# Kernel tuning notes

Hardware: AMD Instinct MI355X
Metric: run time of the kernel (lower is better)

The kernel has to match this reference:

```python
import jax, jax.numpy as jnp
import numpy as np

N_NODES = 100000
N_EDGES = 1600000
IN, HID, OUT = 128, 64, 64


def setup_inputs() -> dict:
    key = jax.random.key(0)
    ks = jax.random.split(key, 7)
    features = jax.random.normal(ks[0], (N_NODES, IN), dtype=jnp.float32)
    src = jax.random.randint(ks[1], (N_EDGES,), 0, N_NODES, dtype=jnp.int64)
    dst = jax.random.randint(ks[2], (N_EDGES,), 0, N_NODES, dtype=jnp.int64)
    # glorot-uniform-like init for GraphConv weights
    lim1 = np.sqrt(6.0 / (IN + HID)).astype(np.float32)
    lim2 = np.sqrt(6.0 / (HID + OUT)).astype(np.float32)
    W1 = jax.random.uniform(ks[3], (IN, HID), jnp.float32, -lim1, lim1)
    b1 = jnp.zeros((HID,), jnp.float32)
    W2 = jax.random.uniform(ks[4], (HID, OUT), jnp.float32, -lim2, lim2)
    b2 = jnp.zeros((OUT,), jnp.float32)
    return {"features": features, "src": src, "dst": dst,
            "W1": W1, "b1": b1, "W2": W2, "b2": b2}


def _graph_conv(h, W, b, src, dst, out_norm, in_norm, relu, n_nodes):
    # DGL GraphConv, norm='both':
    #   h_src *= outdeg^{-1/2}; aggregate sum over edges; h_dst *= indeg^{-1/2}
    #   W applied before aggregation if in_feats > out_feats (fewer bytes moved)
    h = h * out_norm[:, None]
    if h.shape[1] > W.shape[1]:
        h = h @ W
        agg = jax.ops.segment_sum(h[src], dst, num_segments=n_nodes)
    else:
        agg = jax.ops.segment_sum(h[src], dst, num_segments=n_nodes)
        agg = agg @ W
    out = agg * in_norm[:, None] + b
    return jax.nn.relu(out) if relu else out


def reference(features, src, dst, W1, b1, W2, b2):
    n_nodes = features.shape[0]
    ones = jnp.ones(src.shape[0], features.dtype)
    out_deg = jnp.maximum(jax.ops.segment_sum(ones, src, num_segments=n_nodes), 1.0)
    in_deg = jnp.maximum(jax.ops.segment_sum(ones, dst, num_segments=n_nodes), 1.0)
    out_norm = jax.lax.rsqrt(out_deg)
    in_norm = jax.lax.rsqrt(in_deg)
    h = _graph_conv(features, W1, b1, src, dst, out_norm, in_norm, True, n_nodes)
    # Dropout(0.5) between layers: identity in eval mode
    h = _graph_conv(h, W2, b2, src, dst, out_norm, in_norm, False, n_nodes)
    return h
```

## Files before the change

### kernel.cpp

```cpp
#include <hip/hip_runtime.h>
#include <hip/hip_fp16.h>

#define NCH 64
#define INF 128
#define PAD 64
#define NPART 8
#define HCHUNK 12500
#define HQ 64

using ivec4 = __attribute__((ext_vector_type(4))) int;
using hvec8 = __attribute__((ext_vector_type(8))) _Float16;
using fvec8 = __attribute__((ext_vector_type(8))) float;
using half8 = __attribute__((ext_vector_type(8))) _Float16;
using f32x4 = __attribute__((ext_vector_type(4))) float;

__global__ __launch_bounds__(256) void k_histo(const int* __restrict__ src,
                                               int* __restrict__ ohist, int nE, int nN) {
    __shared__ int cnt[HCHUNK];
    const int p = blockIdx.x & (NPART - 1);
    const int q = blockIdx.x >> 3;
    const int lo = p * HCHUNK;
    const int hi = (lo + HCHUNK < nN) ? lo + HCHUNK : nN;
    for (int i = threadIdx.x; i < HCHUNK; i += 256) cnt[i] = 0;
    __syncthreads();
    const int nE4 = nE >> 2;
    const int b0 = (int)(((long)q * nE4) / HQ);
    const int b1 = (int)(((long)(q + 1) * nE4) / HQ);
    for (int i = b0 + threadIdx.x; i < b1; i += 256) {
        ivec4 s4 = __builtin_nontemporal_load(((const ivec4*)src) + i);
#pragma unroll
        for (int j = 0; j < 4; ++j) {
            int s = s4[j];
            if (s >= lo && s < hi) atomicAdd(&cnt[s - lo], 1);
        }
    }
    if (q == 0 && threadIdx.x < (nE & 3)) {
        int s = src[(nE4 << 2) + threadIdx.x];
        if (s >= lo && s < hi) atomicAdd(&cnt[s - lo], 1);
    }
    __syncthreads();
    int* dstp = ohist + (long)blockIdx.x * HCHUNK;
    for (int i = threadIdx.x; i < HCHUNK; i += 256) dstp[i] = cnt[i];
}

__global__ void k_osum(const int* __restrict__ ohist, float* __restrict__ onorm, int nN) {
    int n = blockIdx.x * blockDim.x + threadIdx.x;
    if (n >= nN) return;
    int p = n / HCHUNK, i = n - p * HCHUNK;
    int s = 0;
#pragma unroll 4
    for (int q = 0; q < HQ; ++q)
        s += ohist[(long)((q << 3) | p) * HCHUNK + i];
    onorm[n] = rsqrtf(fmaxf((float)s, 1.0f));
}

__global__ __launch_bounds__(256) void k_build2(
    const int* __restrict__ src, const int* __restrict__ dst,
    int* __restrict__ indeg, int* __restrict__ ell, int nE, int chunk)
{
    const int part = blockIdx.x & (NPART - 1);
    const int lo = part * chunk;
    const int hi = lo + chunk;
    const int setid = blockIdx.x >> 3;
    const int nset = gridDim.x >> 3;
    const int nE4 = nE >> 2;

    int t = setid * 256 + threadIdx.x;
    int stride = nset * 256;
    for (int i = t; i < nE4; i += stride) {
        ivec4 s4 = __builtin_nontemporal_load(((const ivec4*)src) + i);
        ivec4 d4 = __builtin_nontemporal_load(((const ivec4*)dst) + i);
#pragma unroll
        for (int j = 0; j < 4; ++j) {
            int d = d4[j];
            if (d >= lo && d < hi) {
                int pos = atomicAdd(&indeg[d], 1);
                if (pos < PAD) ell[(long)d * PAD + pos] = s4[j];
            }
        }
    }
    if (setid == 0 && threadIdx.x < (nE & 3)) {
        int e = (nE4 << 2) + threadIdx.x;
        int s = src[e], d = dst[e];
        if (d >= lo && d < hi) {
            int pos = atomicAdd(&indeg[d], 1);
            if (pos < PAD) ell[(long)d * PAD + pos] = s;
        }
    }
}

__global__ __launch_bounds__(256) void k_gemm1m(
    const float* __restrict__ feat, const float* __restrict__ W1,
    const float* __restrict__ onorm, __half* __restrict__ h1, int nN)
{
    const int lane = threadIdx.x & 63;
    const int row_in = lane & 15;
    const int kgrp = lane >> 4;
    half8 bf[4][4];
#pragma unroll
    for (int ks = 0; ks < 4; ++ks)
#pragma unroll
        for (int g = 0; g < 4; ++g) {
            int col = g * 16 + row_in;
#pragma unroll
            for (int j = 0; j < 8; ++j)
                bf[ks][g][j] = (_Float16)W1[(ks * 32 + kgrp * 8 + j) * NCH + col];
        }
    const int nTiles = (nN + 15) >> 4;
    int tile = blockIdx.x * 4 + (threadIdx.x >> 6);
    const int stride = gridDim.x * 4;
    for (; tile < nTiles; tile += stride) {
        const long r0 = (long)tile * 16;
        const long ra = r0 + row_in;
        half8 af[4];
        if (ra < nN) {
#pragma unroll
            for (int ks = 0; ks < 4; ++ks) {
                const float* fp = feat + ra * INF + ks * 32 + kgrp * 8;
                float4 x = *(const float4*)fp;
                float4 y = *(const float4*)(fp + 4);
                af[ks][0] = (_Float16)x.x; af[ks][1] = (_Float16)x.y;
                af[ks][2] = (_Float16)x.z; af[ks][3] = (_Float16)x.w;
                af[ks][4] = (_Float16)y.x; af[ks][5] = (_Float16)y.y;
                af[ks][6] = (_Float16)y.z; af[ks][7] = (_Float16)y.w;
            }
        } else {
#pragma unroll
            for (int ks = 0; ks < 4; ++ks)
#pragma unroll
                for (int j = 0; j < 8; ++j) af[ks][j] = (_Float16)0.0f;
        }
        f32x4 acc[4] = {{0,0,0,0},{0,0,0,0},{0,0,0,0},{0,0,0,0}};
#pragma unroll
        for (int ks = 0; ks < 4; ++ks)
#pragma unroll
            for (int g = 0; g < 4; ++g)
                acc[g] = __builtin_amdgcn_mfma_f32_16x16x32_f16(af[ks], bf[ks][g], acc[g], 0, 0, 0);
#pragma unroll
        for (int j = 0; j < 4; ++j) {
            long r = r0 + kgrp * 4 + j;
            if (r < nN) {
                float on = onorm[r];
#pragma unroll
                for (int g = 0; g < 4; ++g)
                    h1[r * NCH + g * 16 + row_in] = __float2half(acc[g][j] * on);
            }
        }
    }
}

__global__ __launch_bounds__(256) void k_agg1(
    const __half* __restrict__ h1s, const int* __restrict__ indeg,
    const int* __restrict__ ell, const float* __restrict__ onorm,
    const float* __restrict__ b1, __half* __restrict__ h2, int nN)
{
    const int c = threadIdx.x & 7;
    int node = (blockIdx.x << 5) + (threadIdx.x >> 3);
    if (node >= nN) return;
    int n0 = indeg[node];
    int n = (n0 > PAD) ? PAD : n0;
    const int* cols = ell + (long)node * PAD;
    fvec8 acc = {0, 0, 0, 0, 0, 0, 0, 0};
    int i = 0;
    for (; i + 4 <= n; i += 4) {
        int s0 = cols[i], s1 = cols[i + 1], s2 = cols[i + 2], s3 = cols[i + 3];
        hvec8 v0 = ((const hvec8*)h1s)[(long)s0 * 8 + c];
        hvec8 v1 = ((const hvec8*)h1s)[(long)s1 * 8 + c];
        hvec8 v2 = ((const hvec8*)h1s)[(long)s2 * 8 + c];
        hvec8 v3 = ((const hvec8*)h1s)[(long)s3 * 8 + c];
#pragma unroll
        for (int j = 0; j < 8; ++j)
            acc[j] += (float)v0[j] + (float)v1[j] + (float)v2[j] + (float)v3[j];
    }
    for (; i < n; ++i) {
        hvec8 v = ((const hvec8*)h1s)[(long)cols[i] * 8 + c];
#pragma unroll
        for (int j = 0; j < 8; ++j) acc[j] += (float)v[j];
    }
    float inn = rsqrtf(fmaxf((float)n0, 1.0f));
    float onn = onorm[node];
    float4 ba = ((const float4*)b1)[2 * c];
    float4 bb = ((const float4*)b1)[2 * c + 1];
    float bv[8] = {ba.x, ba.y, ba.z, ba.w, bb.x, bb.y, bb.z, bb.w};
    hvec8 st;
#pragma unroll
    for (int j = 0; j < 8; ++j)
        st[j] = (_Float16)(fmaxf(acc[j] * inn + bv[j], 0.0f) * onn);
    ((hvec8*)h2)[(long)node * 8 + c] = st;
}

__global__ __launch_bounds__(256) void k_agg2(
    const __half* __restrict__ h2, const int* __restrict__ indeg,
    const int* __restrict__ ell, __half* __restrict__ agg, int nN)
{
    const int c = threadIdx.x & 7;
    int node = (blockIdx.x << 5) + (threadIdx.x >> 3);
    if (node >= nN) return;
    int n0 = indeg[node];
    int n = (n0 > PAD) ? PAD : n0;
    const int* cols = ell + (long)node * PAD;
    fvec8 acc = {0, 0, 0, 0, 0, 0, 0, 0};
    int i = 0;
    for (; i + 4 <= n; i += 4) {
        int s0 = cols[i], s1 = cols[i + 1], s2 = cols[i + 2], s3 = cols[i + 3];
        hvec8 v0 = ((const hvec8*)h2)[(long)s0 * 8 + c];
        hvec8 v1 = ((const hvec8*)h2)[(long)s1 * 8 + c];
        hvec8 v2 = ((const hvec8*)h2)[(long)s2 * 8 + c];
        hvec8 v3 = ((const hvec8*)h2)[(long)s3 * 8 + c];
#pragma unroll
        for (int j = 0; j < 8; ++j)
            acc[j] += (float)v0[j] + (float)v1[j] + (float)v2[j] + (float)v3[j];
    }
    for (; i < n; ++i) {
        hvec8 v = ((const hvec8*)h2)[(long)cols[i] * 8 + c];
#pragma unroll
        for (int j = 0; j < 8; ++j) acc[j] += (float)v[j];
    }
    hvec8 st;
#pragma unroll
    for (int j = 0; j < 8; ++j) st[j] = (_Float16)acc[j];
    ((hvec8*)agg)[(long)node * 8 + c] = st;
}

__global__ __launch_bounds__(256) void k_gemm2m(
    const __half* __restrict__ agg, const float* __restrict__ W2,
    const int* __restrict__ indeg, const float* __restrict__ b2,
    float* __restrict__ out, int nN)
{
    const int lane = threadIdx.x & 63;
    const int row_in = lane & 15;
    const int kgrp = lane >> 4;
    half8 bf[2][4];
#pragma unroll
    for (int ks = 0; ks < 2; ++ks)
#pragma unroll
        for (int g = 0; g < 4; ++g) {
            int col = g * 16 + row_in;
#pragma unroll
            for (int j = 0; j < 8; ++j)
                bf[ks][g][j] = (_Float16)W2[(ks * 32 + kgrp * 8 + j) * NCH + col];
        }
    float bcol[4];
#pragma unroll
    for (int g = 0; g < 4; ++g) bcol[g] = b2[g * 16 + row_in];
    const int nTiles = (nN + 15) >> 4;
    int tile = blockIdx.x * 4 + (threadIdx.x >> 6);
    const int stride = gridDim.x * 4;
    for (; tile < nTiles; tile += stride) {
        const long r0 = (long)tile * 16;
        const long ra = r0 + row_in;
        half8 af[2];
        if (ra < nN) {
#pragma unroll
            for (int ks = 0; ks < 2; ++ks)
                af[ks] = ((const half8*)agg)[ra * 8 + ks * 4 + kgrp];
        } else {
#pragma unroll
            for (int ks = 0; ks < 2; ++ks)
#pragma unroll
                for (int j = 0; j < 8; ++j) af[ks][j] = (_Float16)0.0f;
        }
        f32x4 acc[4] = {{0,0,0,0},{0,0,0,0},{0,0,0,0},{0,0,0,0}};
#pragma unroll
        for (int ks = 0; ks < 2; ++ks)
#pragma unroll
            for (int g = 0; g < 4; ++g)
                acc[g] = __builtin_amdgcn_mfma_f32_16x16x32_f16(af[ks], bf[ks][g], acc[g], 0, 0, 0);
#pragma unroll
        for (int j = 0; j < 4; ++j) {
            long r = r0 + kgrp * 4 + j;
            if (r < nN) {
                float inn = rsqrtf(fmaxf((float)indeg[r], 1.0f));
#pragma unroll
                for (int g = 0; g < 4; ++g)
                    out[r * NCH + g * 16 + row_in] = acc[g][j] * inn + bcol[g];
            }
        }
    }
}

extern "C" void kernel_launch(void* const* d_in, const int* in_sizes, int n_in,
                              void* d_out, int out_size, void* d_ws, size_t ws_size,
                              hipStream_t stream) {
    const float* feat = (const float*)d_in[0];
    const int* src    = (const int*)d_in[1];
    const int* dst    = (const int*)d_in[2];
    const float* W1   = (const float*)d_in[3];
    const float* b1   = (const float*)d_in[4];
    const float* W2   = (const float*)d_in[5];
    const float* b2   = (const float*)d_in[6];
    float* out        = (float*)d_out;

    const int nN = in_sizes[0] / INF;
    const int nE = in_sizes[1];
    const int chunk = (nN + NPART - 1) / NPART;

    char* p = (char*)d_ws;
    float* onorm  = (float*)p;   p += (size_t)nN * 4;
    int* indeg    = (int*)p;     p += (size_t)nN * 4;
    char* unionp  = p;           p += (size_t)nN * NCH * 2 * 2;
    int* ell      = (int*)p;     p += (size_t)nN * PAD * 4;
    int* ohist    = (int*)unionp;
    __half* h2    = (__half*)unionp;
    __half* agg2  = (__half*)(unionp + (size_t)nN * NCH * 2);
    __half* h1    = (__half*)d_out;

    (void)hipMemsetAsync(indeg, 0, (size_t)nN * 4, stream);

    k_histo<<<NPART * HQ, 256, 0, stream>>>(src, ohist, nE, nN);
    k_osum<<<(nN + 255) / 256, 256, 0, stream>>>(ohist, onorm, nN);

    k_gemm1m<<<512, 256, 0, stream>>>(feat, W1, onorm, h1, nN);

    k_build2<<<2048, 256, 0, stream>>>(src, dst, indeg, ell, nE, chunk);

    k_agg1<<<(nN + 31) / 32, 256, 0, stream>>>(h1, indeg, ell, onorm, b1, h2, nN);

    k_agg2<<<(nN + 31) / 32, 256, 0, stream>>>(h2, indeg, ell, agg2, nN);

    k_gemm2m<<<512, 256, 0, stream>>>(agg2, W2, indeg, b2, out, nN);
}
```

Before: 207.5 us.

## Build ELL adjacency via per-chunk LDS histograms and prefix offsets instead of global atomics

Replaces the global-atomic ELL build with a two-pass scheme: packed 16-bit LDS histograms for src and dst per edge chunk, a per-node exclusive scan over chunks that also produces the degree norm and in-degree, then a fill kernel that places edges using LDS atomics seeded with the chunk offsets. This removes global atomics on indeg and the memset. The cost is an extra dst histogram pass and a scan kernel. The 16-bit packed counters could overflow only for very high-degree nodes.

```diff
diff --git a/kernel.cpp b/kernel.cpp
--- a/kernel.cpp
+++ b/kernel.cpp
@@ -4,9 +4,11 @@
 #define NCH 64
 #define INF 128
 #define PAD 64
-#define NPART 8
-#define HCHUNK 12500
 #define HQ 64
+#define NPH 4
+#define CHUNK_H 25000
+#define NPF 8
+#define CHUNK_F 12500
 
 using ivec4 = __attribute__((ext_vector_type(4))) int;
 using hvec8 = __attribute__((ext_vector_type(8))) _Float16;
@@ -14,77 +16,91 @@
 using half8 = __attribute__((ext_vector_type(8))) _Float16;
 using f32x4 = __attribute__((ext_vector_type(4))) float;
 
-__global__ __launch_bounds__(256) void k_histo(const int* __restrict__ src,
-                                               int* __restrict__ ohist, int nE, int nN) {
-    __shared__ int cnt[HCHUNK];
-    const int p = blockIdx.x & (NPART - 1);
+__global__ __launch_bounds__(256) void k_hist(const int* __restrict__ arr,
+                                              unsigned* __restrict__ hist, int nE, int nN) {
+    __shared__ unsigned cnt[CHUNK_H / 2];
+    const int p = blockIdx.x & (NPH - 1);
+    const int q = blockIdx.x >> 2;
+    const int lo = p * CHUNK_H;
+    for (int i = threadIdx.x; i < CHUNK_H / 2; i += 256) cnt[i] = 0;
+    __syncthreads();
+    const int nE4 = nE >> 2;
+    const int b0 = (int)(((long)q * nE4) / HQ);
+    const int b1 = (int)(((long)(q + 1) * nE4) / HQ);
+    for (int i = b0 + threadIdx.x; i < b1; i += 256) {
+        ivec4 v4 = __builtin_nontemporal_load(((const ivec4*)arr) + i);
+#pragma unroll
+        for (int j = 0; j < 4; ++j) {
+            int x = v4[j] - lo;
+            if ((unsigned)x < (unsigned)CHUNK_H)
+                atomicAdd(&cnt[x >> 1], 1u << ((x & 1) * 16));
+        }
+    }
+    if (q == 0 && threadIdx.x < (nE & 3)) {
+        int x = arr[(nE4 << 2) + threadIdx.x] - lo;
+        if ((unsigned)x < (unsigned)CHUNK_H)
+            atomicAdd(&cnt[x >> 1], 1u << ((x & 1) * 16));
+    }
+    __syncthreads();
+    unsigned* hp = hist + (long)q * (nN >> 1) + p * (CHUNK_H / 2);
+    int lim = nN - lo;
+    if (lim > CHUNK_H) lim = CHUNK_H;
+    lim >>= 1;
+    for (int i = threadIdx.x; i < lim; i += 256) hp[i] = cnt[i];
+}
+
+__global__ void k_scan2(const unsigned short* __restrict__ shist,
+                        unsigned short* __restrict__ dhist,
+                        float* __restrict__ onorm, int* __restrict__ indeg, int nN) {
+    int n = blockIdx.x * blockDim.x + threadIdx.x;
+    if (n >= nN) return;
+    int s = 0;
+#pragma unroll 4
+    for (int q = 0; q < HQ; ++q) s += shist[(long)q * nN + n];
+    onorm[n] = rsqrtf(fmaxf((float)s, 1.0f));
+    int run = 0;
+    for (int q = 0; q < HQ; ++q) {
+        long idx = (long)q * nN + n;
+        int v = dhist[idx];
+        dhist[idx] = (unsigned short)run;
+        run += v;
+    }
+    indeg[n] = run;
+}
+
+__global__ __launch_bounds__(256) void k_fill(
+    const int* __restrict__ src, const int* __restrict__ dst,
+    const unsigned short* __restrict__ qoff, int* __restrict__ ell, int nE, int nN) {
+    __shared__ int cnt[CHUNK_F];
+    const int p = blockIdx.x & (NPF - 1);
     const int q = blockIdx.x >> 3;
-    const int lo = p * HCHUNK;
-    const int hi = (lo + HCHUNK < nN) ? lo + HCHUNK : nN;
-    for (int i = threadIdx.x; i < HCHUNK; i += 256) cnt[i] = 0;
+    const int lo = p * CHUNK_F;
+    for (int i = threadIdx.x; i < CHUNK_F; i += 256) {
+        int n = lo + i;
+        cnt[i] = (n < nN) ? (int)qoff[(long)q * nN + n] : 0;
+    }
     __syncthreads();
     const int nE4 = nE >> 2;
     const int b0 = (int)(((long)q * nE4) / HQ);
     const int b1 = (int)(((long)(q + 1) * nE4) / HQ);
     for (int i = b0 + threadIdx.x; i < b1; i += 256) {
         ivec4 s4 = __builtin_nontemporal_load(((const ivec4*)src) + i);
+        ivec4 d4 = __builtin_nontemporal_load(((const ivec4*)dst) + i);
 #pragma unroll
         for (int j = 0; j < 4; ++j) {
-            int s = s4[j];
-            if (s >= lo && s < hi) atomicAdd(&cnt[s - lo], 1);
+            int d = d4[j] - lo;
+            if ((unsigned)d < (unsigned)CHUNK_F) {
+                int pos = atomicAdd(&cnt[d], 1);
+                if (pos < PAD) ell[(long)(lo + d) * PAD + pos] = s4[j];
+            }
         }
     }
     if (q == 0 && threadIdx.x < (nE & 3)) {
-        int s = src[(nE4 << 2) + threadIdx.x];
-        if (s >= lo && s < hi) atomicAdd(&cnt[s - lo], 1);
-    }
-    __syncthreads();
-    int* dstp = ohist + (long)blockIdx.x * HCHUNK;
-    for (int i = threadIdx.x; i < HCHUNK; i += 256) dstp[i] = cnt[i];
-}
-
-__global__ void k_osum(const int* __restrict__ ohist, float* __restrict__ onorm, int nN) {
-    int n = blockIdx.x * blockDim.x + threadIdx.x;
-    if (n >= nN) return;
-    int p = n / HCHUNK, i = n - p * HCHUNK;
-    int s = 0;
-#pragma unroll 4
-    for (int q = 0; q < HQ; ++q)
-        s += ohist[(long)((q << 3) | p) * HCHUNK + i];
-    onorm[n] = rsqrtf(fmaxf((float)s, 1.0f));
-}
-
-__global__ __launch_bounds__(256) void k_build2(
-    const int* __restrict__ src, const int* __restrict__ dst,
-    int* __restrict__ indeg, int* __restrict__ ell, int nE, int chunk)
-{
-    const int part = blockIdx.x & (NPART - 1);
-    const int lo = part * chunk;
-    const int hi = lo + chunk;
-    const int setid = blockIdx.x >> 3;
-    const int nset = gridDim.x >> 3;
-    const int nE4 = nE >> 2;
-
-    int t = setid * 256 + threadIdx.x;
-    int stride = nset * 256;
-    for (int i = t; i < nE4; i += stride) {
-        ivec4 s4 = __builtin_nontemporal_load(((const ivec4*)src) + i);
-        ivec4 d4 = __builtin_nontemporal_load(((const ivec4*)dst) + i);
-#pragma unroll
-        for (int j = 0; j < 4; ++j) {
-            int d = d4[j];
-            if (d >= lo && d < hi) {
-                int pos = atomicAdd(&indeg[d], 1);
-                if (pos < PAD) ell[(long)d * PAD + pos] = s4[j];
-            }
-        }
-    }
-    if (setid == 0 && threadIdx.x < (nE & 3)) {
         int e = (nE4 << 2) + threadIdx.x;
-        int s = src[e], d = dst[e];
-        if (d >= lo && d < hi) {
-            int pos = atomicAdd(&indeg[d], 1);
-            if (pos < PAD) ell[(long)d * PAD + pos] = s;
+        int d = dst[e] - lo;
+        if ((unsigned)d < (unsigned)CHUNK_F) {
+            int pos = atomicAdd(&cnt[d], 1);
+            if (pos < PAD) ell[(long)(lo + d) * PAD + pos] = src[e];
         }
     }
 }
@@ -293,26 +309,27 @@
 
     const int nN = in_sizes[0] / INF;
     const int nE = in_sizes[1];
-    const int chunk = (nN + NPART - 1) / NPART;
 
     char* p = (char*)d_ws;
     float* onorm  = (float*)p;   p += (size_t)nN * 4;
     int* indeg    = (int*)p;     p += (size_t)nN * 4;
     char* unionp  = p;           p += (size_t)nN * NCH * 2 * 2;
     int* ell      = (int*)p;     p += (size_t)nN * PAD * 4;
-    int* ohist    = (int*)unionp;
+    unsigned* shist = (unsigned*)unionp;
+    unsigned* dhist = (unsigned*)(unionp + (size_t)HQ * nN * 2);
     __half* h2    = (__half*)unionp;
     __half* agg2  = (__half*)(unionp + (size_t)nN * NCH * 2);
     __half* h1    = (__half*)d_out;
 
-    (void)hipMemsetAsync(indeg, 0, (size_t)nN * 4, stream);
-
-    k_histo<<<NPART * HQ, 256, 0, stream>>>(src, ohist, nE, nN);
-    k_osum<<<(nN + 255) / 256, 256, 0, stream>>>(ohist, onorm, nN);
+    k_hist<<<NPH * HQ, 256, 0, stream>>>(src, shist, nE, nN);
+    k_hist<<<NPH * HQ, 256, 0, stream>>>(dst, dhist, nE, nN);
+
+    k_scan2<<<(nN + 255) / 256, 256, 0, stream>>>((const unsigned short*)shist,
+                                                  (unsigned short*)dhist, onorm, indeg, nN);
 
     k_gemm1m<<<512, 256, 0, stream>>>(feat, W1, onorm, h1, nN);
 
-    k_build2<<<2048, 256, 0, stream>>>(src, dst, indeg, ell, nE, chunk);
+    k_fill<<<NPF * HQ, 256, 0, stream>>>(src, dst, (const unsigned short*)dhist, ell, nE, nN);
 
     k_agg1<<<(nN + 31) / 32, 256, 0, stream>>>(h1, indeg, ell, onorm, b1, h2, nN);
 
```

After: 202.4 us. 1.03x faster.
